# Kernel optimization log

Measured on AMD Instinct MI355X. Metric: run time of the kernel, lower is better.

The kernel has to match this reference:

```python
import jax, jax.numpy as jnp
import numpy as np

D = 1024
H = 16
DH = D // H
FF = 4096
EPS = 1e-5


def _layernorm(x, g, b):
    m = jnp.mean(x, axis=-1, keepdims=True)
    v = jnp.mean(jnp.square(x - m), axis=-1, keepdims=True)
    return (x - m) * jax.lax.rsqrt(v + EPS) * g + b


def setup_inputs() -> dict:
    key = jax.random.key(0)
    ks = jax.random.split(key, 24)
    B, S = 2, 2048
    s = 0.02
    inp = {
        "tokens": jax.random.normal(ks[0], (B, S, D), jnp.float32),
        "attention_bias": jax.random.normal(ks[1], (B, S, S, 3), jnp.float32),
        "metadata_compatibility": jax.random.normal(ks[2], (B, S, S), jnp.float32),
        "key_padding_mask": jnp.zeros((B, S), jnp.bool_),
        "ln1_g": jnp.ones((D,), jnp.float32),
        "ln1_b": jnp.zeros((D,), jnp.float32),
        "Wq": jax.random.normal(ks[3], (D, D), jnp.float32) * s,
        "bq": jnp.zeros((D,), jnp.float32),
        "Wk": jax.random.normal(ks[4], (D, D), jnp.float32) * s,
        "bk": jnp.zeros((D,), jnp.float32),
        "Wv": jax.random.normal(ks[5], (D, D), jnp.float32) * s,
        "bv": jnp.zeros((D,), jnp.float32),
        "Wo": jax.random.normal(ks[6], (D, D), jnp.float32) * s,
        "bo": jnp.zeros((D,), jnp.float32),
        "Ws": jax.random.normal(ks[7], (3, H), jnp.float32) * s,
        "bs": jnp.zeros((H,), jnp.float32),
        "Wm": jax.random.normal(ks[8], (1, H), jnp.float32) * s,
        "bm": jnp.zeros((H,), jnp.float32),
        "ln2_g": jnp.ones((D,), jnp.float32),
        "ln2_b": jnp.zeros((D,), jnp.float32),
        "W1": jax.random.normal(ks[9], (D, FF), jnp.float32) * s,
        "b1": jnp.zeros((FF,), jnp.float32),
        "W2": jax.random.normal(ks[10], (FF, D), jnp.float32) * s,
        "b2": jnp.zeros((D,), jnp.float32),
    }
    return inp


def reference(tokens, attention_bias, metadata_compatibility, key_padding_mask,
              ln1_g, ln1_b, Wq, bq, Wk, bk, Wv, bv, Wo, bo,
              Ws, bs, Wm, bm, ln2_g, ln2_b, W1, b1, W2, b2):
    B, S, _ = tokens.shape
    scale = DH ** -0.5
    n = _layernorm(tokens, ln1_g, ln1_b)
    # project and split heads: [B,S,H,DH]
    q = (n @ Wq + bq).reshape(B, S, H, DH)
    k = (n @ Wk + bk).reshape(B, S, H, DH)
    v = (n @ Wv + bv).reshape(B, S, H, DH)
    logits = jnp.einsum('bihd,bjhd->bhij', q, k) * scale  # [B,H,S,S]
    # structural bias: Linear(3->H) then permute to [B,H,S,S]
    logits = logits + jnp.einsum('bijc,ch->bhij', attention_bias, Ws) + bs[None, :, None, None]
    # metadata bias: Linear(1->H)
    logits = logits + metadata_compatibility[:, None, :, :] * Wm[0][None, :, None, None] + bm[None, :, None, None]
    logits = jnp.where(key_padding_mask[:, None, None, :], -1e9, logits)
    w = jax.nn.softmax(logits, axis=-1)
    attended = jnp.einsum('bhij,bjhd->bihd', w, v).reshape(B, S, D)
    x = tokens + (attended @ Wo + bo)
    h = _layernorm(x, ln2_g, ln2_b)
    ff = jax.nn.gelu(h @ W1 + b1, approximate=False) @ W2 + b2
    return x + ff
```

## Files before the change

kernel.cpp:

```cpp
#include <hip/hip_runtime.h>

#define S_LEN 2048
#define DMODEL 1024
#define NH 16
#define DH 64
#define FFDIM 4096

typedef __bf16 bf16x8 __attribute__((ext_vector_type(8)));
typedef float f32x4 __attribute__((ext_vector_type(4)));
typedef unsigned short ushort_t;

#define AS1 __attribute__((address_space(1)))
#define AS3 __attribute__((address_space(3)))

__device__ __forceinline__ void gll16(const void* g, void* l) {
  __builtin_amdgcn_global_load_lds((AS1 const void*)g, (AS3 void*)l, 16, 0, 0);
}

__device__ __forceinline__ unsigned short f2b(float f){
  unsigned u = __builtin_bit_cast(unsigned, f);
  u = (u + 0x7FFFu + ((u >> 16) & 1u)) >> 16;
  return (unsigned short)u;
}

__device__ __forceinline__ float b2f(unsigned short us){
  return __builtin_bit_cast(float, (unsigned)us << 16);
}

__device__ __forceinline__ unsigned cvt_pk_bf16(float lo, float hi){
  unsigned r;
  asm("v_cvt_pk_bf16_f32 %0, %1, %2" : "=v"(r) : "v"(lo), "v"(hi));
  return r;
}

__device__ __forceinline__ float gelu_exact(float x){
  return 0.5f * x * (1.0f + erff(x * 0.70710678118654752f));
}

__device__ __forceinline__ f32x4 mfma16(bf16x8 a, bf16x8 b, f32x4 c){
  return __builtin_amdgcn_mfma_f32_16x16x32_bf16(a, b, c, 0, 0, 0);
}

__global__ __launch_bounds__(256) void tconv6(
    const float* __restrict__ s0, const float* __restrict__ s1,
    const float* __restrict__ s2, const float* __restrict__ s3,
    const float* __restrict__ s4, const float* __restrict__ s5,
    ushort_t* __restrict__ d0, ushort_t* __restrict__ d1,
    ushort_t* __restrict__ d2, ushort_t* __restrict__ d3,
    ushort_t* __restrict__ d4, ushort_t* __restrict__ d5)
{
  __shared__ float tile[32][33];
  int bx = blockIdx.x;
  const float* W; ushort_t* Wt; int K, N, n0, k0;
  if (bx < 4096) {
    int seg = bx >> 10, t_ = bx & 1023;
    W = (seg == 0) ? s0 : (seg == 1) ? s1 : (seg == 2) ? s2 : s3;
    Wt = (seg == 0) ? d0 : (seg == 1) ? d1 : (seg == 2) ? d2 : d3;
    K = 1024; N = 1024; n0 = (t_ & 31) * 32; k0 = (t_ >> 5) * 32;
  } else if (bx < 8192) {
    int t_ = bx - 4096;
    W = s4; Wt = d4; K = 1024; N = 4096;
    n0 = (t_ & 127) * 32; k0 = (t_ >> 7) * 32;
  } else {
    int t_ = bx - 8192;
    W = s5; Wt = d5; K = 4096; N = 1024;
    n0 = (t_ & 31) * 32; k0 = (t_ >> 5) * 32;
  }
  int tx = threadIdx.x, ty = threadIdx.y;
#pragma unroll
  for (int i = 0; i < 4; ++i)
    tile[ty + i*8][tx] = W[(size_t)(k0 + ty + i*8) * N + n0 + tx];
  __syncthreads();
#pragma unroll
  for (int i = 0; i < 4; ++i)
    Wt[(size_t)(n0 + ty + i*8) * K + k0 + tx] = f2b(tile[tx][ty + i*8]);
}

__global__ __launch_bounds__(256) void ln_kernel(
    const float* __restrict__ x, const float* __restrict__ g,
    const float* __restrict__ bt, ushort_t* __restrict__ out)
{
  int row = blockIdx.x;
  int t = threadIdx.x;
  const float4 v = *(const float4*)&x[(size_t)row * DMODEL + t * 4];
  float s = v.x + v.y + v.z + v.w;
  float s2 = v.x*v.x + v.y*v.y + v.z*v.z + v.w*v.w;
#pragma unroll
  for (int d = 1; d < 64; d <<= 1) {
    s  += __shfl_xor(s,  d, 64);
    s2 += __shfl_xor(s2, d, 64);
  }
  __shared__ float red[8];
  int w = t >> 6;
  if ((t & 63) == 0) { red[w] = s; red[4 + w] = s2; }
  __syncthreads();
  s  = red[0] + red[1] + red[2] + red[3];
  s2 = red[4] + red[5] + red[6] + red[7];
  float mean = s * (1.0f / DMODEL);
  float var  = s2 * (1.0f / DMODEL) - mean * mean;
  float rstd = rsqrtf(var + 1e-5f);
  float4 gg = *(const float4*)&g[t * 4];
  float4 bb = *(const float4*)&bt[t * 4];
  ushort4 o;
  o.x = f2b((v.x - mean) * rstd * gg.x + bb.x);
  o.y = f2b((v.y - mean) * rstd * gg.y + bb.y);
  o.z = f2b((v.z - mean) * rstd * gg.z + bb.z);
  o.w = f2b((v.w - mean) * rstd * gg.w + bb.w);
  *(ushort4*)&out[(size_t)row * DMODEL + t * 4] = o;
}

__global__ __launch_bounds__(256) void bias_head_kernel(
    const float* __restrict__ ab, const float* __restrict__ mc,
    const unsigned char* __restrict__ kp,
    const float* __restrict__ Ws, const float* __restrict__ bs,
    const float* __restrict__ Wm, const float* __restrict__ bm,
    ushort_t* __restrict__ bp)
{
  int bi = blockIdx.x;
  int b = bi >> 11;
  int i = bi & (S_LEN - 1);
  int t = threadIdx.x;
  int j0 = t * 8;
  float av[24];
  const float4* A4 = (const float4*)(ab + ((size_t)bi * S_LEN + j0) * 3);
#pragma unroll
  for (int u = 0; u < 6; ++u) {
    float4 x = A4[u];
    av[u*4] = x.x; av[u*4+1] = x.y; av[u*4+2] = x.z; av[u*4+3] = x.w;
  }
  float mv[8];
  const float4* M4 = (const float4*)(mc + (size_t)bi * S_LEN + j0);
#pragma unroll
  for (int u = 0; u < 2; ++u) {
    float4 x = M4[u];
    mv[u*4] = x.x; mv[u*4+1] = x.y; mv[u*4+2] = x.z; mv[u*4+3] = x.w;
  }
  unsigned long long kq = *(const unsigned long long*)(kp + (size_t)b * S_LEN + j0);
#pragma unroll
  for (int h = 0; h < NH; ++h) {
    float w0 = Ws[h], w1 = Ws[NH + h], w2 = Ws[2*NH + h];
    float wm = Wm[h], cc = bs[h] + bm[h];
    float v[8];
#pragma unroll
    for (int j = 0; j < 8; ++j) {
      float vv = av[j*3]*w0 + av[j*3+1]*w1 + av[j*3+2]*w2 + mv[j]*wm + cc;
      if ((kq >> (8*j)) & 1ull) vv = -1e9f;
      v[j] = vv;
    }
    uint4 pk;
    pk.x = cvt_pk_bf16(v[0], v[1]);
    pk.y = cvt_pk_bf16(v[2], v[3]);
    pk.z = cvt_pk_bf16(v[4], v[5]);
    pk.w = cvt_pk_bf16(v[6], v[7]);
    *(uint4*)&bp[((size_t)(b*NH + h) * S_LEN + i) * S_LEN + j0] = pk;
  }
}

template<int MODE>
__global__ __launch_bounds__(256) void gemm_bt(
    const ushort_t* __restrict__ A, const ushort_t* __restrict__ Bt,
    const float* __restrict__ b0p, const float* __restrict__ b1p,
    const float* __restrict__ b2p,
    void* __restrict__ o0, void* __restrict__ o1, void* __restrict__ o2,
    int M, int N, int K)
{
  __shared__ ushort_t sh[2][8192];
  int t = threadIdx.x;
  int m0 = blockIdx.y * 128, n0 = blockIdx.x * 128;
  int w = t >> 6, l = t & 63, lr = l & 15, lg = l >> 4;
  int wr = (w >> 1) * 64, wc = (w & 1) * 64;

  const ushort_t* srcp[4];
  int dsto[4];
#pragma unroll
  for (int j = 0; j < 4; ++j) {
    int c = j * 4 + w;
    int o = c * 1024 + l * 16;
    if (c < 8)
      srcp[j] = &A[(size_t)(m0 + (o >> 6)) * K + ((o & 63) >> 1)];
    else {
      int o2 = o - 8192;
      srcp[j] = &Bt[(size_t)(n0 + (o2 >> 6)) * K + ((o2 & 63) >> 1)];
    }
    dsto[j] = o;
  }

#define GSTAGE(bi, kk) do { \
  _Pragma("unroll") \
  for (int j = 0; j < 4; ++j) gll16(srcp[j] + (kk), (char*)sh[bi] + dsto[j]); \
} while (0)

  GSTAGE(0, 0);
  __syncthreads();
  f32x4 acc[4][4] = {};
  int cur = 0;
  for (int k0 = 0; k0 < K; k0 += 32) {
    if (k0 + 32 < K) GSTAGE(cur ^ 1, k0 + 32);
    const ushort_t* s = sh[cur];
    bf16x8 af[4], bfr[4];
#pragma unroll
    for (int a = 0; a < 4; ++a)
      af[a] = *(const bf16x8*)&s[(wr + a * 16 + lr) * 32 + lg * 8];
#pragma unroll
    for (int b = 0; b < 4; ++b)
      bfr[b] = *(const bf16x8*)&s[4096 + (wc + b * 16 + lr) * 32 + lg * 8];
    __builtin_amdgcn_s_setprio(1);
#pragma unroll
    for (int a = 0; a < 4; ++a)
#pragma unroll
      for (int b = 0; b < 4; ++b)
        acc[a][b] = mfma16(af[a], bfr[b], acc[a][b]);
    __builtin_amdgcn_s_setprio(0);
    __syncthreads();
    cur ^= 1;
  }
#undef GSTAGE

  if (MODE == 3) {
    ushort_t* out = (ushort_t*)o0;
#pragma unroll
    for (int a = 0; a < 4; ++a)
#pragma unroll
      for (int b = 0; b < 4; ++b) {
        int gn = n0 + wc + b * 16 + lr;
        float bv = b0p[gn];
#pragma unroll
        for (int r = 0; r < 4; ++r) {
          int gm = m0 + wr + a * 16 + lg * 4 + r;
          out[(size_t)gm * N + gn] = f2b(gelu_exact(acc[a][b][r] + bv));
        }
      }
  } else {
    int seg = n0 >> 10;
    int nb0 = n0 & 1023;
    const float* bi = (seg == 0) ? b0p : (seg == 1) ? b1p : b2p;
    if (seg < 2) {
      ushort_t* out = (ushort_t*)((seg == 0) ? o0 : o1);
#pragma unroll
      for (int a = 0; a < 4; ++a)
#pragma unroll
        for (int b = 0; b < 4; ++b) {
          int nn = nb0 + wc + b * 16 + lr;
          float bv = bi[nn];
#pragma unroll
          for (int r = 0; r < 4; ++r) {
            int gm = m0 + wr + a * 16 + lg * 4 + r;
            out[(size_t)gm * DMODEL + nn] = f2b(acc[a][b][r] + bv);
          }
        }
    } else {
      ushort_t* out = (ushort_t*)o2;
#pragma unroll
      for (int a = 0; a < 4; ++a)
#pragma unroll
        for (int b = 0; b < 4; ++b) {
          int nn = nb0 + wc + b * 16 + lr;
          int gm = m0 + wr + a * 16 + lg * 4;
          float bv = bi[nn];
          ushort4 pk;
          pk.x = f2b(acc[a][b][0] + bv);
          pk.y = f2b(acc[a][b][1] + bv);
          pk.z = f2b(acc[a][b][2] + bv);
          pk.w = f2b(acc[a][b][3] + bv);
          size_t addr = (((size_t)(gm >> 11) * NH + (nn >> 6)) * DH + (nn & 63)) * S_LEN
                        + (gm & (S_LEN - 1));
          *(ushort4*)&out[addr] = pk;
        }
    }
  }
}

__global__ __launch_bounds__(256) void gemm64_res(
    const ushort_t* __restrict__ A, const ushort_t* __restrict__ Bt,
    const float* __restrict__ bias, const float* __restrict__ res,
    float* __restrict__ out, int M, int N, int K)
{
  __shared__ ushort_t sh[2][6144];
  int t = threadIdx.x;
  int m0 = blockIdx.y * 128, n0 = blockIdx.x * 64;
  int w = t >> 6, l = t & 63, lr = l & 15, lg = l >> 4;
  int wr = (w >> 1) * 64, wc = (w & 1) * 32;

  const ushort_t* srcp[3];
  int dsto[3];
#pragma unroll
  for (int j = 0; j < 3; ++j) {
    int c = j * 4 + w;
    int o = c * 1024 + l * 16;
    if (c < 8)
      srcp[j] = &A[(size_t)(m0 + (o >> 6)) * K + ((o & 63) >> 1)];
    else {
      int o2 = o - 8192;
      srcp[j] = &Bt[(size_t)(n0 + (o2 >> 6)) * K + ((o2 & 63) >> 1)];
    }
    dsto[j] = o;
  }

#define GSTAGE64(bi, kk) do { \
  _Pragma("unroll") \
  for (int j = 0; j < 3; ++j) gll16(srcp[j] + (kk), (char*)sh[bi] + dsto[j]); \
} while (0)

  GSTAGE64(0, 0);
  __syncthreads();
  f32x4 acc[4][2] = {};
  int cur = 0;
  for (int k0 = 0; k0 < K; k0 += 32) {
    if (k0 + 32 < K) GSTAGE64(cur ^ 1, k0 + 32);
    const ushort_t* s = sh[cur];
    bf16x8 af[4], bfr[2];
#pragma unroll
    for (int a = 0; a < 4; ++a)
      af[a] = *(const bf16x8*)&s[(wr + a * 16 + lr) * 32 + lg * 8];
#pragma unroll
    for (int b = 0; b < 2; ++b)
      bfr[b] = *(const bf16x8*)&s[4096 + (wc + b * 16 + lr) * 32 + lg * 8];
    __builtin_amdgcn_s_setprio(1);
#pragma unroll
    for (int a = 0; a < 4; ++a)
#pragma unroll
      for (int b = 0; b < 2; ++b)
        acc[a][b] = mfma16(af[a], bfr[b], acc[a][b]);
    __builtin_amdgcn_s_setprio(0);
    __syncthreads();
    cur ^= 1;
  }
#undef GSTAGE64

#pragma unroll
  for (int a = 0; a < 4; ++a)
#pragma unroll
    for (int b = 0; b < 2; ++b) {
      int gn = n0 + wc + b * 16 + lr;
      float bv = bias[gn];
#pragma unroll
      for (int r = 0; r < 4; ++r) {
        int gm = m0 + wr + a * 16 + lg * 4 + r;
        out[(size_t)gm * N + gn] = acc[a][b][r] + bv + res[(size_t)gm * N + gn];
      }
    }
}

__global__ __launch_bounds__(256) void attn_kernel(
    const ushort_t* __restrict__ q, const ushort_t* __restrict__ k,
    const ushort_t* __restrict__ vt, const ushort_t* __restrict__ bp,
    ushort_t* __restrict__ att)
{
  __shared__ ushort_t kbuf[2][4096];
  __shared__ ushort_t vbuf[2][4096];
  __shared__ ushort_t p_lds[4096];
  int bh = blockIdx.y;
  int b = bh >> 4, h = bh & 15;
  int i0 = blockIdx.x * 64;
  int t = threadIdx.x, w = t >> 6, l = t & 63;
  int lr = l & 15, lg = l >> 4;
  int rho = lr & 7;
  const float scale = 0.125f;

  int srow0 = t >> 3, srow1 = 32 + (t >> 3);
  int c16 = t & 7;
  size_t kb0 = (size_t)b * S_LEN * DMODEL + h * DH;
  size_t vb0 = (size_t)(b * NH + h) * DH * S_LEN;
  size_t koff0 = (size_t)srow0 * DMODEL + ((c16 ^ (srow0 & 7)) << 3);
  size_t koff1 = (size_t)srow1 * DMODEL + ((c16 ^ (srow1 & 7)) << 3);
  size_t voff0 = (size_t)srow0 * S_LEN + ((c16 ^ (srow0 & 7)) << 3);
  size_t voff1 = (size_t)srow1 * S_LEN + ((c16 ^ (srow1 & 7)) << 3);
  int do0 = t * 8, do1 = 2048 + t * 8;

#define STAGE_KV(bi, j0_) do { \
  size_t kr = kb0 + (size_t)(j0_) * DMODEL; \
  size_t vr = vb0 + (size_t)(j0_); \
  gll16(k + kr + koff0, &kbuf[bi][do0]); \
  gll16(k + kr + koff1, &kbuf[bi][do1]); \
  gll16(vt + vr + voff0, &vbuf[bi][do0]); \
  gll16(vt + vr + voff1, &vbuf[bi][do1]); \
} while (0)

  int qrow = i0 + w * 16 + lr;
  size_t qbase = (size_t)(b * S_LEN + qrow) * DMODEL + h * DH;
  bf16x8 aq0 = *(const bf16x8*)&q[qbase + lg * 8];
  bf16x8 aq1 = *(const bf16x8*)&q[qbase + 32 + lg * 8];

  size_t rbias = ((size_t)bh * S_LEN + qrow) * S_LEN;

  f32x4 acc_o[4] = {};
  float m_run = -1e30f, l_run = 0.0f;

  STAGE_KV(0, 0);
  __syncthreads();

  for (int jt = 0; jt < S_LEN / 64; ++jt) {
    int cur = jt & 1;
    if (jt + 1 < S_LEN / 64) STAGE_KV(cur ^ 1, (jt + 1) * 64);

    const char* kbc = (const char*)kbuf[cur];
    f32x4 acc_s[4] = {};
    __builtin_amdgcn_s_setprio(1);
#pragma unroll
    for (int n = 0; n < 4; ++n) {
      const char* rb = kbc + (n * 16 + lr) * 128;
      bf16x8 k0 = *(const bf16x8*)(rb + ((lg ^ rho) << 4));
      bf16x8 k1 = *(const bf16x8*)(rb + (((4 + lg) ^ rho) << 4));
      acc_s[n] = mfma16(k0, aq0, acc_s[n]);
      acc_s[n] = mfma16(k1, aq1, acc_s[n]);
    }
    __builtin_amdgcn_s_setprio(0);

    float p[16];
#pragma unroll
    for (int n = 0; n < 4; ++n) {
      uint2 raw = *(const uint2*)&bp[rbias + jt * 64 + n * 16 + lg * 4];
      p[n*4+0] = fmaf(acc_s[n][0], scale, b2f((unsigned short)(raw.x & 0xFFFF)));
      p[n*4+1] = fmaf(acc_s[n][1], scale, b2f((unsigned short)(raw.x >> 16)));
      p[n*4+2] = fmaf(acc_s[n][2], scale, b2f((unsigned short)(raw.y & 0xFFFF)));
      p[n*4+3] = fmaf(acc_s[n][3], scale, b2f((unsigned short)(raw.y >> 16)));
    }
    float t8[8], t4[4];
#pragma unroll
    for (int i = 0; i < 8; ++i) t8[i] = fmaxf(p[i], p[i + 8]);
#pragma unroll
    for (int i = 0; i < 4; ++i) t4[i] = fmaxf(t8[i], t8[i + 4]);
    float mx = fmaxf(fmaxf(t4[0], t4[1]), fmaxf(t4[2], t4[3]));
    mx = fmaxf(mx, __shfl_xor(mx, 16, 64));
    mx = fmaxf(mx, __shfl_xor(mx, 32, 64));
    float mnew = fmaxf(m_run, mx);
    float sf = __expf(m_run - mnew);
    m_run = mnew;
#pragma unroll
    for (int i = 0; i < 16; ++i) p[i] = __expf(p[i] - mnew);
    float s8[8], s4[4];
#pragma unroll
    for (int i = 0; i < 8; ++i) s8[i] = p[i] + p[i + 8];
#pragma unroll
    for (int i = 0; i < 4; ++i) s4[i] = s8[i] + s8[i + 4];
    float ls = (s4[0] + s4[1]) + (s4[2] + s4[3]);
    ls += __shfl_xor(ls, 16, 64);
    ls += __shfl_xor(ls, 32, 64);
    l_run = l_run * sf + ls;

    float sfr[4];
#pragma unroll
    for (int r = 0; r < 4; ++r) sfr[r] = __shfl(sf, lg * 4 + r, 64);
#pragma unroll
    for (int nd = 0; nd < 4; ++nd)
#pragma unroll
      for (int r = 0; r < 4; ++r) acc_o[nd][r] *= sfr[r];

    char* pb = (char*)p_lds + (w * 16 + lr) * 128;
#pragma unroll
    for (int n = 0; n < 4; ++n) {
      uint2 pk2;
      pk2.x = cvt_pk_bf16(p[n*4+0], p[n*4+1]);
      pk2.y = cvt_pk_bf16(p[n*4+2], p[n*4+3]);
      *(uint2*)(pb + ((n * 32 + lg * 8) ^ (rho << 4))) = pk2;
    }
    asm volatile("s_waitcnt lgkmcnt(0)" ::: "memory");
    __builtin_amdgcn_sched_barrier(0);

    bf16x8 ap0 = *(const bf16x8*)(pb + ((lg ^ rho) << 4));
    bf16x8 ap1 = *(const bf16x8*)(pb + (((4 + lg) ^ rho) << 4));
    const char* vbc = (const char*)vbuf[cur];
    __builtin_amdgcn_s_setprio(1);
#pragma unroll
    for (int nd = 0; nd < 4; ++nd) {
      const char* rb = vbc + (nd * 16 + lr) * 128;
      bf16x8 v0 = *(const bf16x8*)(rb + ((lg ^ rho) << 4));
      bf16x8 v1 = *(const bf16x8*)(rb + (((4 + lg) ^ rho) << 4));
      acc_o[nd] = mfma16(ap0, v0, acc_o[nd]);
      acc_o[nd] = mfma16(ap1, v1, acc_o[nd]);
    }
    __builtin_amdgcn_s_setprio(0);
    __syncthreads();
  }
#undef STAGE_KV

  float inv[4];
#pragma unroll
  for (int r = 0; r < 4; ++r) inv[r] = 1.0f / __shfl(l_run, lg * 4 + r, 64);
#pragma unroll
  for (int r = 0; r < 4; ++r) {
    int gr = i0 + w * 16 + lg * 4 + r;
#pragma unroll
    for (int nd = 0; nd < 4; ++nd)
      att[(size_t)(b * S_LEN + gr) * DMODEL + h * DH + nd * 16 + lr] =
          f2b(acc_o[nd][r] * inv[r]);
  }
}

extern "C" void kernel_launch(void* const* d_in, const int* in_sizes, int n_in,
                              void* d_out, int out_size, void* d_ws, size_t ws_size,
                              hipStream_t stream) {
  const float* tokens = (const float*)d_in[0];
  const float* ab     = (const float*)d_in[1];
  const float* mc     = (const float*)d_in[2];
  const unsigned char* kp = (const unsigned char*)d_in[3];
  const float* ln1g = (const float*)d_in[4];
  const float* ln1b = (const float*)d_in[5];
  const float* Wq = (const float*)d_in[6];
  const float* bq = (const float*)d_in[7];
  const float* Wk = (const float*)d_in[8];
  const float* bk = (const float*)d_in[9];
  const float* Wv = (const float*)d_in[10];
  const float* bv = (const float*)d_in[11];
  const float* Wo = (const float*)d_in[12];
  const float* bo = (const float*)d_in[13];
  const float* Ws = (const float*)d_in[14];
  const float* bs = (const float*)d_in[15];
  const float* Wm = (const float*)d_in[16];
  const float* bm = (const float*)d_in[17];
  const float* ln2g = (const float*)d_in[18];
  const float* ln2b = (const float*)d_in[19];
  const float* W1 = (const float*)d_in[20];
  const float* b1 = (const float*)d_in[21];
  const float* W2 = (const float*)d_in[22];
  const float* b2 = (const float*)d_in[23];
  float* out = (float*)d_out;

  int B = in_sizes[0] / (S_LEN * DMODEL);
  int M = B * S_LEN;

  char* ws = (char*)d_ws;
  ushort_t* nb  = (ushort_t*)(ws + 0);
  ushort_t* qb  = (ushort_t*)(ws + (size_t)8388608);
  ushort_t* kb  = (ushort_t*)(ws + (size_t)16777216);
  ushort_t* vtb = (ushort_t*)(ws + (size_t)25165824);
  ushort_t* ff1 = (ushort_t*)(ws + 0);
  ushort_t* wt_q = (ushort_t*)(ws + (size_t)33554432);
  ushort_t* wt_k = (ushort_t*)(ws + (size_t)35651584);
  ushort_t* wt_v = (ushort_t*)(ws + (size_t)37748736);
  ushort_t* wt_o = (ushort_t*)(ws + (size_t)39845888);
  ushort_t* wt_1 = (ushort_t*)(ws + (size_t)41943040);
  ushort_t* wt_2 = (ushort_t*)(ws + (size_t)50331648);
  ushort_t* attb = (ushort_t*)(ws + (size_t)58720256);
  float*    xb   = (float*)   (ws + (size_t)67108864);
  ushort_t* hb   = (ushort_t*)(ws + (size_t)83886080);
  ushort_t* bp   = (ushort_t*)(ws + (size_t)92274688);

  tconv6<<<12288, dim3(32, 8), 0, stream>>>(Wq, Wk, Wv, Wo, W1, W2,
                                            wt_q, wt_k, wt_v, wt_o, wt_1, wt_2);

  ln_kernel<<<M, 256, 0, stream>>>(tokens, ln1g, ln1b, nb);

  bias_head_kernel<<<M, 256, 0, stream>>>(ab, mc, kp, Ws, bs, Wm, bm, bp);

  gemm_bt<4><<<dim3(24, M / 128), 256, 0, stream>>>(
      nb, wt_q, bq, bk, bv, qb, kb, vtb, M, 3 * DMODEL, DMODEL);

  attn_kernel<<<dim3(S_LEN / 64, B * NH), 256, 0, stream>>>(qb, kb, vtb, bp, attb);

  gemm64_res<<<dim3(16, M / 128), 256, 0, stream>>>(
      attb, wt_o, bo, tokens, xb, M, DMODEL, DMODEL);

  ln_kernel<<<M, 256, 0, stream>>>(xb, ln2g, ln2b, hb);

  gemm_bt<3><<<dim3(32, M / 128), 256, 0, stream>>>(
      hb, wt_1, b1, nullptr, nullptr, ff1, nullptr, nullptr, M, FFDIM, DMODEL);

  gemm64_res<<<dim3(16, M / 128), 256, 0, stream>>>(
      ff1, wt_2, b2, xb, out, M, DMODEL, FFDIM);
}
```

Measured before the change: 643.9 us.

## Prefetch attention bias, lazily rescale softmax, widen weight transpose tiles

The attention kernel now loads the next tile's bias values into registers one iteration ahead, so their global-load latency overlaps the current tile's compute. It also skips the running-max update and the rescaling of the output accumulator whenever every lane's new max stays within 8 of the current max, which removes exponentials and shuffles on most iterations. The weight transpose/convert kernel moves to 64x64 tiles with float4 loads and 16-byte stores, cutting block count and widening memory transactions. Lazy rescaling allows exponentials up to about e^8 before renormalising, and the bias prefetch adds register pressure.

```diff
diff --git a/kernel.cpp b/kernel.cpp
--- a/kernel.cpp
+++ b/kernel.cpp
@@ -41,7 +41,7 @@
   return __builtin_amdgcn_mfma_f32_16x16x32_bf16(a, b, c, 0, 0, 0);
 }
 
-__global__ __launch_bounds__(256) void tconv6(
+__global__ __launch_bounds__(256) void tconv64(
     const float* __restrict__ s0, const float* __restrict__ s1,
     const float* __restrict__ s2, const float* __restrict__ s3,
     const float* __restrict__ s4, const float* __restrict__ s5,
@@ -49,31 +49,40 @@
     ushort_t* __restrict__ d2, ushort_t* __restrict__ d3,
     ushort_t* __restrict__ d4, ushort_t* __restrict__ d5)
 {
-  __shared__ float tile[32][33];
+  __shared__ float tile[64][65];
   int bx = blockIdx.x;
   const float* W; ushort_t* Wt; int K, N, n0, k0;
-  if (bx < 4096) {
-    int seg = bx >> 10, t_ = bx & 1023;
-    W = (seg == 0) ? s0 : (seg == 1) ? s1 : (seg == 2) ? s2 : s3;
+  if (bx < 1024) {
+    int seg = bx >> 8, t_ = bx & 255;
+    W  = (seg == 0) ? s0 : (seg == 1) ? s1 : (seg == 2) ? s2 : s3;
     Wt = (seg == 0) ? d0 : (seg == 1) ? d1 : (seg == 2) ? d2 : d3;
-    K = 1024; N = 1024; n0 = (t_ & 31) * 32; k0 = (t_ >> 5) * 32;
-  } else if (bx < 8192) {
-    int t_ = bx - 4096;
+    K = 1024; N = 1024; n0 = (t_ & 15) * 64; k0 = (t_ >> 4) * 64;
+  } else if (bx < 2048) {
+    int t_ = bx - 1024;
     W = s4; Wt = d4; K = 1024; N = 4096;
-    n0 = (t_ & 127) * 32; k0 = (t_ >> 7) * 32;
+    n0 = (t_ & 63) * 64; k0 = (t_ >> 6) * 64;
   } else {
-    int t_ = bx - 8192;
+    int t_ = bx - 2048;
     W = s5; Wt = d5; K = 4096; N = 1024;
-    n0 = (t_ & 31) * 32; k0 = (t_ >> 5) * 32;
-  }
-  int tx = threadIdx.x, ty = threadIdx.y;
-#pragma unroll
-  for (int i = 0; i < 4; ++i)
-    tile[ty + i*8][tx] = W[(size_t)(k0 + ty + i*8) * N + n0 + tx];
+    n0 = (t_ & 15) * 64; k0 = (t_ >> 4) * 64;
+  }
+  int t = threadIdx.x;
+  int lrow = t >> 4, lcol = (t & 15) * 4;
+#pragma unroll
+  for (int i = 0; i < 4; ++i) {
+    float4 v = *(const float4*)&W[(size_t)(k0 + lrow + i * 16) * N + n0 + lcol];
+    tile[lrow + i * 16][lcol]     = v.x;
+    tile[lrow + i * 16][lcol + 1] = v.y;
+    tile[lrow + i * 16][lcol + 2] = v.z;
+    tile[lrow + i * 16][lcol + 3] = v.w;
+  }
   __syncthreads();
-#pragma unroll
-  for (int i = 0; i < 4; ++i)
-    Wt[(size_t)(n0 + ty + i*8) * K + k0 + tx] = f2b(tile[tx][ty + i*8]);
+  int orow = t >> 2, oseg = (t & 3) * 16;
+  alignas(16) ushort_t ob[16];
+#pragma unroll
+  for (int j = 0; j < 16; ++j) ob[j] = f2b(tile[oseg + j][orow]);
+  *(uint4*)&Wt[(size_t)(n0 + orow) * K + k0 + oseg]     = *(const uint4*)ob;
+  *(uint4*)&Wt[(size_t)(n0 + orow) * K + k0 + oseg + 8] = *((const uint4*)ob + 1);
 }
 
 __global__ __launch_bounds__(256) void ln_kernel(
@@ -118,7 +127,6 @@
 {
   int bi = blockIdx.x;
   int b = bi >> 11;
-  int i = bi & (S_LEN - 1);
   int t = threadIdx.x;
   int j0 = t * 8;
   float av[24];
@@ -152,7 +160,7 @@
     pk.y = cvt_pk_bf16(v[2], v[3]);
     pk.z = cvt_pk_bf16(v[4], v[5]);
     pk.w = cvt_pk_bf16(v[6], v[7]);
-    *(uint4*)&bp[((size_t)(b*NH + h) * S_LEN + i) * S_LEN + j0] = pk;
+    *(uint4*)&bp[((size_t)(b*NH + h) * S_LEN + (bi & (S_LEN-1))) * S_LEN + j0] = pk;
   }
 }
 
@@ -356,6 +364,7 @@
   int lr = l & 15, lg = l >> 4;
   int rho = lr & 7;
   const float scale = 0.125f;
+  const int NT = S_LEN / 64;
 
   int srow0 = t >> 3, srow1 = 32 + (t >> 3);
   int c16 = t & 7;
@@ -381,17 +390,28 @@
   bf16x8 aq0 = *(const bf16x8*)&q[qbase + lg * 8];
   bf16x8 aq1 = *(const bf16x8*)&q[qbase + 32 + lg * 8];
 
-  size_t rbias = ((size_t)bh * S_LEN + qrow) * S_LEN;
+  const ushort_t* bprow = bp + ((size_t)bh * S_LEN + qrow) * S_LEN + lg * 4;
 
   f32x4 acc_o[4] = {};
   float m_run = -1e30f, l_run = 0.0f;
 
+  uint2 braw[4];
+#pragma unroll
+  for (int n = 0; n < 4; ++n) braw[n] = *(const uint2*)(bprow + n * 16);
+
   STAGE_KV(0, 0);
   __syncthreads();
 
-  for (int jt = 0; jt < S_LEN / 64; ++jt) {
+  for (int jt = 0; jt < NT; ++jt) {
     int cur = jt & 1;
-    if (jt + 1 < S_LEN / 64) STAGE_KV(cur ^ 1, (jt + 1) * 64);
+    if (jt + 1 < NT) STAGE_KV(cur ^ 1, (jt + 1) * 64);
+
+    uint2 bn[4] = {braw[0], braw[1], braw[2], braw[3]};
+    if (jt + 1 < NT) {
+      const ushort_t* bpt = bprow + (jt + 1) * 64;
+#pragma unroll
+      for (int n = 0; n < 4; ++n) bn[n] = *(const uint2*)(bpt + n * 16);
+    }
 
     const char* kbc = (const char*)kbuf[cur];
     f32x4 acc_s[4] = {};
@@ -409,11 +429,10 @@
     float p[16];
 #pragma unroll
     for (int n = 0; n < 4; ++n) {
-      uint2 raw = *(const uint2*)&bp[rbias + jt * 64 + n * 16 + lg * 4];
-      p[n*4+0] = fmaf(acc_s[n][0], scale, b2f((unsigned short)(raw.x & 0xFFFF)));
-      p[n*4+1] = fmaf(acc_s[n][1], scale, b2f((unsigned short)(raw.x >> 16)));
-      p[n*4+2] = fmaf(acc_s[n][2], scale, b2f((unsigned short)(raw.y & 0xFFFF)));
-      p[n*4+3] = fmaf(acc_s[n][3], scale, b2f((unsigned short)(raw.y >> 16)));
+      p[n*4+0] = fmaf(acc_s[n][0], scale, b2f((unsigned short)(braw[n].x & 0xFFFF)));
+      p[n*4+1] = fmaf(acc_s[n][1], scale, b2f((unsigned short)(braw[n].x >> 16)));
+      p[n*4+2] = fmaf(acc_s[n][2], scale, b2f((unsigned short)(braw[n].y & 0xFFFF)));
+      p[n*4+3] = fmaf(acc_s[n][3], scale, b2f((unsigned short)(braw[n].y >> 16)));
     }
     float t8[8], t4[4];
 #pragma unroll
@@ -423,11 +442,22 @@
     float mx = fmaxf(fmaxf(t4[0], t4[1]), fmaxf(t4[2], t4[3]));
     mx = fmaxf(mx, __shfl_xor(mx, 16, 64));
     mx = fmaxf(mx, __shfl_xor(mx, 32, 64));
-    float mnew = fmaxf(m_run, mx);
-    float sf = __expf(m_run - mnew);
-    m_run = mnew;
-#pragma unroll
-    for (int i = 0; i < 16; ++i) p[i] = __expf(p[i] - mnew);
+
+    if (!__all(mx <= m_run + 8.0f)) {
+      float mnew = fmaxf(m_run, mx);
+      float sf = __expf(m_run - mnew);
+      m_run = mnew;
+      l_run *= sf;
+      float sfr[4];
+#pragma unroll
+      for (int r = 0; r < 4; ++r) sfr[r] = __shfl(sf, lg * 4 + r, 64);
+#pragma unroll
+      for (int nd = 0; nd < 4; ++nd)
+#pragma unroll
+        for (int r = 0; r < 4; ++r) acc_o[nd][r] *= sfr[r];
+    }
+#pragma unroll
+    for (int i = 0; i < 16; ++i) p[i] = __expf(p[i] - m_run);
     float s8[8], s4[4];
 #pragma unroll
     for (int i = 0; i < 8; ++i) s8[i] = p[i] + p[i + 8];
@@ -436,15 +466,7 @@
     float ls = (s4[0] + s4[1]) + (s4[2] + s4[3]);
     ls += __shfl_xor(ls, 16, 64);
     ls += __shfl_xor(ls, 32, 64);
-    l_run = l_run * sf + ls;
-
-    float sfr[4];
-#pragma unroll
-    for (int r = 0; r < 4; ++r) sfr[r] = __shfl(sf, lg * 4 + r, 64);
-#pragma unroll
-    for (int nd = 0; nd < 4; ++nd)
-#pragma unroll
-      for (int r = 0; r < 4; ++r) acc_o[nd][r] *= sfr[r];
+    l_run += ls;
 
     char* pb = (char*)p_lds + (w * 16 + lr) * 128;
 #pragma unroll
@@ -471,6 +493,8 @@
     }
     __builtin_amdgcn_s_setprio(0);
     __syncthreads();
+#pragma unroll
+    for (int n = 0; n < 4; ++n) braw[n] = bn[n];
   }
 #undef STAGE_KV
 
@@ -536,8 +560,8 @@
   ushort_t* hb   = (ushort_t*)(ws + (size_t)83886080);
   ushort_t* bp   = (ushort_t*)(ws + (size_t)92274688);
 
-  tconv6<<<12288, dim3(32, 8), 0, stream>>>(Wq, Wk, Wv, Wo, W1, W2,
-                                            wt_q, wt_k, wt_v, wt_o, wt_1, wt_2);
+  tconv64<<<3072, 256, 0, stream>>>(Wq, Wk, Wv, Wo, W1, W2,
+                                    wt_q, wt_k, wt_v, wt_o, wt_1, wt_2);
 
   ln_kernel<<<M, 256, 0, stream>>>(tokens, ln1g, ln1b, nb);
 
```

New measurement: 636.4 us. No clear change (-1.2%).
